# Optimization experiments

Measured on AMD Instinct MI355X. Metric: run time of the kernel, lower is better.

## Reference

```python
import jax, jax.numpy as jnp
import numpy as np

IN_FEATURES = 4096
OUT_FEATURES = 4096
N_GROUPS = 32
GROUP_SIZE = IN_FEATURES // N_GROUPS  # 128


def setup_inputs() -> dict:
    key = jax.random.key(0)
    k_x, k_qw, k_s, k_zp, k_b = jax.random.split(key, 5)
    x = jax.random.normal(k_x, (2, 2048, IN_FEATURES), dtype=jnp.float32)
    # 4-bit GPTQ quantized weight values in [0, 16)
    qweight_int = jax.random.randint(k_qw, (IN_FEATURES, OUT_FEATURES), 0, 16, dtype=jnp.int32)
    scales = jax.random.uniform(k_s, (N_GROUPS, OUT_FEATURES), dtype=jnp.float32, minval=0.001, maxval=0.02)
    zero_points = jax.random.randint(k_zp, (N_GROUPS, OUT_FEATURES), 0, 16, dtype=jnp.int32)
    # standard (non-permuted) g_idx: group index per input channel
    g_idx = (jnp.arange(IN_FEATURES, dtype=jnp.int32) // GROUP_SIZE).astype(jnp.int32)
    bias = jax.random.normal(k_b, (OUT_FEATURES,), dtype=jnp.float32)
    return {"x": x, "qweight_int": qweight_int, "scales": scales,
            "zero_points": zero_points, "g_idx": g_idx, "bias": bias}


def reference(x, qweight_int, scales, zero_points, g_idx, bias):
    dtype = x.dtype
    gi = g_idx.astype(jnp.int32)
    # dequantize: W[i, o] = scales[g_idx[i], o] * (q[i, o] - zp[g_idx[i], o])
    qw = qweight_int.astype(dtype)                       # [in, out]
    zp = zero_points.astype(dtype)[gi]                   # [in, out] via gather
    sc = scales.astype(dtype)[gi]                        # [in, out] via gather
    weight = sc * (qw - zp)                              # [in, out]
    out_shape = x.shape[:-1] + (qweight_int.shape[1],)
    x2d = x.reshape(-1, x.shape[-1])                     # [tokens, in]
    out = (x2d @ weight).reshape(out_shape)              # [b, s, out]
    out = out + bias.astype(dtype)
    return out
```

## Files before the change

### kernel.cpp

```cpp
#include <hip/hip_runtime.h>
#include <hip/hip_bf16.h>

typedef int  int4v  __attribute__((ext_vector_type(4)));
typedef int  int16v __attribute__((ext_vector_type(16)));

#define M_DIM 4096
#define N_DIM 4096
#define K_DIM 4096
#define NG 32
#define GS 128

__global__ void prep_kernel(const float* __restrict__ x,
                            signed char* __restrict__ xq,
                            float* __restrict__ sx,
                            const int* __restrict__ qw,
                            const int* __restrict__ zps,
                            signed char* __restrict__ wq) {
    __shared__ float red[4];
    __shared__ float inv_s;
    const int tid = threadIdx.x;
    if (blockIdx.x < 4096) {
        const int m = blockIdx.x;
        const float4* xr = reinterpret_cast<const float4*>(x + (long)m * K_DIM);
        float4 v[4];
        float amax = 0.f;
#pragma unroll
        for (int j = 0; j < 4; ++j) {
            v[j] = xr[tid * 4 + j];
            amax = fmaxf(amax, fmaxf(fmaxf(fabsf(v[j].x), fabsf(v[j].y)),
                                     fmaxf(fabsf(v[j].z), fabsf(v[j].w))));
        }
#pragma unroll
        for (int off = 32; off >= 1; off >>= 1)
            amax = fmaxf(amax, __shfl_xor(amax, off));
        if ((tid & 63) == 0) red[tid >> 6] = amax;
        __syncthreads();
        if (tid == 0) {
            float a = fmaxf(fmaxf(red[0], red[1]), fmaxf(red[2], red[3]));
            sx[m] = a * (1.f / 127.f);
            inv_s = (a > 0.f) ? 127.f / a : 0.f;
        }
        __syncthreads();
        const float inv = inv_s;
        unsigned p[4];
#pragma unroll
        for (int j = 0; j < 4; ++j) {
            int a0 = __float2int_rn(v[j].x * inv);
            int a1 = __float2int_rn(v[j].y * inv);
            int a2 = __float2int_rn(v[j].z * inv);
            int a3 = __float2int_rn(v[j].w * inv);
            p[j] = (a0 & 255) | ((a1 & 255) << 8) | ((a2 & 255) << 16) | ((a3 & 255) << 24);
        }
        *reinterpret_cast<uint4*>(xq + (long)m * K_DIM + tid * 16) =
            make_uint4(p[0], p[1], p[2], p[3]);
        return;
    }
    const int bx = blockIdx.x - 4096;
    const int n0 = (bx & 63) * 64;
    const int k0 = (bx >> 6) * 64;
    const int g  = k0 >> 7;
    const int n  = tid & 63;
    const int w  = tid >> 6;
    const int zp = zps[g * N_DIM + n0 + n];
    const int kk = k0 + w * 16;
    unsigned p[4];
#pragma unroll
    for (int c = 0; c < 4; ++c) {
        unsigned acc = 0;
#pragma unroll
        for (int j = 0; j < 4; ++j) {
            int q = qw[(long)(kk + c * 4 + j) * N_DIM + n0 + n];
            acc |= (unsigned)((q - zp) & 255) << (8 * j);
        }
        p[c] = acc;
    }
    *reinterpret_cast<uint4*>(wq + (long)(n0 + n) * K_DIM + kk) =
        make_uint4(p[0], p[1], p[2], p[3]);
}

#define BM 256
#define BN 128
#define BK 128

__device__ __forceinline__ void async_ld16(const signed char* g, const signed char* l) {
    __builtin_amdgcn_global_load_lds(
        (const __attribute__((address_space(1))) void*)g,
        (__attribute__((address_space(3))) void*)l, 16, 0, 0);
}

__global__ __launch_bounds__(256, 2) void gemm_kernel(
    const signed char* __restrict__ A,
    const signed char* __restrict__ Bq,
    const float* __restrict__ scales,
    const float* __restrict__ sx,
    const float* __restrict__ bias,
    float* __restrict__ C) {
    __shared__ signed char As[BM * BK];
    __shared__ signed char Bs[BN * BK];
    __shared__ float sS[NG * BN];
    __shared__ float sxs[BM];
    const int tid  = threadIdx.x;
    const int wave = tid >> 6;
    const int lane = tid & 63;
    const int half = lane >> 5;
    const int l32  = lane & 31;
    const int wm = (wave >> 1) * 128;
    const int wn = (wave & 1) * 64;
    const int m0 = blockIdx.y * BM;
    const int n0 = blockIdx.x * BN;

#pragma unroll
    for (int j = 0; j < 16; j += 4) {
        int i = tid * 16 + j;
        *reinterpret_cast<float4*>(&sS[i]) =
            *reinterpret_cast<const float4*>(&scales[(i >> 7) * N_DIM + n0 + (i & 127)]);
    }
    sxs[tid] = sx[m0 + tid];

    const int srow  = tid >> 3;
    const int sunit = (tid & 7) ^ (srow & 7);
    const signed char* agp = A  + (long)(m0 + srow) * K_DIM + sunit * 16;
    const signed char* bgp = Bq + (long)(n0 + srow) * K_DIM + sunit * 16;

    float facc[4][2][16];
#pragma unroll
    for (int mt = 0; mt < 4; ++mt)
#pragma unroll
        for (int nt = 0; nt < 2; ++nt)
#pragma unroll
            for (int r = 0; r < 16; ++r) facc[mt][nt][r] = 0.f;
    int16v zero16;
#pragma unroll
    for (int r = 0; r < 16; ++r) zero16[r] = 0;

    for (int kk = 0; kk < K_DIM; kk += BK) {
#pragma unroll
        for (int p = 0; p < 8; ++p)
            async_ld16(agp + (long)p * 32 * K_DIM + kk, As + p * 4096 + wave * 1024);
#pragma unroll
        for (int p = 0; p < 4; ++p)
            async_ld16(bgp + (long)p * 32 * K_DIM + kk, Bs + p * 4096 + wave * 1024);
        __syncthreads();
        const int g = kk >> 7;
        const float s0 = sS[g * BN + wn + l32];
        const float s1 = sS[g * BN + wn + 32 + l32];
        int4v bf[2][4];
#pragma unroll
        for (int nt = 0; nt < 2; ++nt) {
            int n = wn + nt * 32 + l32;
#pragma unroll
            for (int ks = 0; ks < 4; ++ks) {
                int slot = (2 * ks + half) ^ (n & 7);
                bf[nt][ks] = *reinterpret_cast<const int4v*>(&Bs[n * BK + slot * 16]);
            }
        }
#pragma unroll
        for (int mt = 0; mt < 4; ++mt) {
            int m = wm + mt * 32 + l32;
            int4v af[4];
#pragma unroll
            for (int ks = 0; ks < 4; ++ks) {
                int slot = (2 * ks + half) ^ (m & 7);
                af[ks] = *reinterpret_cast<const int4v*>(&As[m * BK + slot * 16]);
            }
            int16v c0 = __builtin_amdgcn_mfma_i32_32x32x32_i8(af[0], bf[0][0], zero16, 0, 0, 0);
            int16v c1 = __builtin_amdgcn_mfma_i32_32x32x32_i8(af[0], bf[1][0], zero16, 0, 0, 0);
#pragma unroll
            for (int ks = 1; ks < 4; ++ks) {
                c0 = __builtin_amdgcn_mfma_i32_32x32x32_i8(af[ks], bf[0][ks], c0, 0, 0, 0);
                c1 = __builtin_amdgcn_mfma_i32_32x32x32_i8(af[ks], bf[1][ks], c1, 0, 0, 0);
            }
#pragma unroll
            for (int r = 0; r < 16; ++r) {
                facc[mt][0][r] += s0 * (float)c0[r];
                facc[mt][1][r] += s1 * (float)c1[r];
            }
        }
        __syncthreads();
    }

    float bv[2];
    bv[0] = bias[n0 + wn + l32];
    bv[1] = bias[n0 + wn + 32 + l32];
    const int rowh = half * 4;
#pragma unroll
    for (int mt = 0; mt < 4; ++mt) {
#pragma unroll
        for (int r = 0; r < 16; ++r) {
            int row = (r & 3) + 8 * (r >> 2) + rowh;
            int gm  = m0 + wm + mt * 32 + row;
            float sxm = sxs[wm + mt * 32 + row];
            float* crow = C + (long)gm * N_DIM + n0 + wn;
            crow[l32]      = facc[mt][0][r] * sxm + bv[0];
            crow[32 + l32] = facc[mt][1][r] * sxm + bv[1];
        }
    }
}

extern "C" void kernel_launch(void* const* d_in, const int* in_sizes, int n_in,
                              void* d_out, int out_size, void* d_ws, size_t ws_size,
                              hipStream_t stream) {
    const float* x      = (const float*)d_in[0];
    const int*   qw     = (const int*)d_in[1];
    const float* scales = (const float*)d_in[2];
    const int*   zps    = (const int*)d_in[3];
    const float* bias   = (const float*)d_in[5];
    float* out = (float*)d_out;

    signed char* xq = (signed char*)d_ws;
    signed char* wq = (signed char*)d_ws + (size_t)M_DIM * K_DIM;
    float*       sx = (float*)((signed char*)d_ws + 2 * (size_t)M_DIM * K_DIM);

    prep_kernel<<<8192, 256, 0, stream>>>(x, xq, sx, qw, zps, wq);
    gemm_kernel<<<dim3(N_DIM / BN, M_DIM / BM), 256, 0, stream>>>(
        xq, wq, scales, sx, bias, out);
}
```

Baseline: 266.1 us.

## Double-buffer LDS tiles in 256x256 int8 GEMM with 512 threads and block swizzle

The int8 GEMM tile grows from 256x128 to 256x256 with 8 waves per block, and the A/B tiles are double-buffered in LDS so the async global-to-LDS loads for the next K step overlap the MFMA work on the current one. Per-group scales and the per-row activation scales are now read straight from global memory (scales prefetched one iteration ahead) instead of being staged in shared memory. Block indices are swizzled for L2 locality. LDS use rises to 128KB and occupancy drops to one block per CU, which trades latency hiding through concurrent blocks for deeper in-block pipelining. The prep kernel is unchanged and still accounts for part of the total time.

New measurement: 266.2 us. About the same (+0.0%).

```diff
diff --git a/kernel.cpp b/kernel.cpp
--- a/kernel.cpp
+++ b/kernel.cpp
@@ -79,8 +79,9 @@
 }
 
 #define BM 256
-#define BN 128
+#define BN 256
 #define BK 128
+#define NT (K_DIM / BK)
 
 __device__ __forceinline__ void async_ld16(const signed char* g, const signed char* l) {
     __builtin_amdgcn_global_load_lds(
@@ -88,39 +89,44 @@
         (__attribute__((address_space(3))) void*)l, 16, 0, 0);
 }
 
-__global__ __launch_bounds__(256, 2) void gemm_kernel(
+__device__ __forceinline__ void stage_tiles(const signed char* agp, const signed char* bgp,
+                                            signed char* asb, signed char* bsb,
+                                            int wave, int kk) {
+#pragma unroll
+    for (int p = 0; p < 4; ++p)
+        async_ld16(agp + (long)(p * 64) * K_DIM + kk, asb + p * 8192 + wave * 1024);
+#pragma unroll
+    for (int p = 0; p < 4; ++p)
+        async_ld16(bgp + (long)(p * 64) * K_DIM + kk, bsb + p * 8192 + wave * 1024);
+}
+
+__global__ __launch_bounds__(512, 1) void gemm_kernel(
     const signed char* __restrict__ A,
     const signed char* __restrict__ Bq,
     const float* __restrict__ scales,
     const float* __restrict__ sx,
     const float* __restrict__ bias,
     float* __restrict__ C) {
-    __shared__ signed char As[BM * BK];
-    __shared__ signed char Bs[BN * BK];
-    __shared__ float sS[NG * BN];
-    __shared__ float sxs[BM];
+    __shared__ signed char As[2][BM * BK];
+    __shared__ signed char Bs[2][BN * BK];
     const int tid  = threadIdx.x;
     const int wave = tid >> 6;
     const int lane = tid & 63;
     const int half = lane >> 5;
     const int l32  = lane & 31;
-    const int wm = (wave >> 1) * 128;
-    const int wn = (wave & 1) * 64;
-    const int m0 = blockIdx.y * BM;
-    const int n0 = blockIdx.x * BN;
-
-#pragma unroll
-    for (int j = 0; j < 16; j += 4) {
-        int i = tid * 16 + j;
-        *reinterpret_cast<float4*>(&sS[i]) =
-            *reinterpret_cast<const float4*>(&scales[(i >> 7) * N_DIM + n0 + (i & 127)]);
-    }
-    sxs[tid] = sx[m0 + tid];
+    const int wm = (wave >> 2) * 128;
+    const int wn = (wave & 3) * 64;
+
+    const int bid = (int)blockIdx.x;
+    const int swz = (bid & 7) * 32 + (bid >> 3);
+    const int m0 = (swz >> 4) * BM;
+    const int n0 = (swz & 15) * BN;
 
     const int srow  = tid >> 3;
     const int sunit = (tid & 7) ^ (srow & 7);
     const signed char* agp = A  + (long)(m0 + srow) * K_DIM + sunit * 16;
     const signed char* bgp = Bq + (long)(n0 + srow) * K_DIM + sunit * 16;
+    const float* sp = scales + n0 + wn + l32;
 
     float facc[4][2][16];
 #pragma unroll
@@ -133,17 +139,22 @@
 #pragma unroll
     for (int r = 0; r < 16; ++r) zero16[r] = 0;
 
-    for (int kk = 0; kk < K_DIM; kk += BK) {
-#pragma unroll
-        for (int p = 0; p < 8; ++p)
-            async_ld16(agp + (long)p * 32 * K_DIM + kk, As + p * 4096 + wave * 1024);
-#pragma unroll
-        for (int p = 0; p < 4; ++p)
-            async_ld16(bgp + (long)p * 32 * K_DIM + kk, Bs + p * 4096 + wave * 1024);
-        __syncthreads();
-        const int g = kk >> 7;
-        const float s0 = sS[g * BN + wn + l32];
-        const float s1 = sS[g * BN + wn + 32 + l32];
+    stage_tiles(agp, bgp, As[0], Bs[0], wave, 0);
+    float s0 = sp[0];
+    float s1 = sp[32];
+    __syncthreads();
+
+    for (int t = 0; t < NT; ++t) {
+        if (t + 1 < NT)
+            stage_tiles(agp, bgp, As[(t + 1) & 1], Bs[(t + 1) & 1], wave, (t + 1) * BK);
+        float ns0 = 0.f, ns1 = 0.f;
+        if (t + 1 < NT) {
+            ns0 = sp[(long)(t + 1) * N_DIM];
+            ns1 = sp[(long)(t + 1) * N_DIM + 32];
+        }
+
+        const signed char* Ab = As[t & 1];
+        const signed char* Bb = Bs[t & 1];
         int4v bf[2][4];
 #pragma unroll
         for (int nt = 0; nt < 2; ++nt) {
@@ -151,7 +162,7 @@
 #pragma unroll
             for (int ks = 0; ks < 4; ++ks) {
                 int slot = (2 * ks + half) ^ (n & 7);
-                bf[nt][ks] = *reinterpret_cast<const int4v*>(&Bs[n * BK + slot * 16]);
+                bf[nt][ks] = *reinterpret_cast<const int4v*>(&Bb[n * BK + slot * 16]);
             }
         }
 #pragma unroll
@@ -161,7 +172,7 @@
 #pragma unroll
             for (int ks = 0; ks < 4; ++ks) {
                 int slot = (2 * ks + half) ^ (m & 7);
-                af[ks] = *reinterpret_cast<const int4v*>(&As[m * BK + slot * 16]);
+                af[ks] = *reinterpret_cast<const int4v*>(&Ab[m * BK + slot * 16]);
             }
             int16v c0 = __builtin_amdgcn_mfma_i32_32x32x32_i8(af[0], bf[0][0], zero16, 0, 0, 0);
             int16v c1 = __builtin_amdgcn_mfma_i32_32x32x32_i8(af[0], bf[1][0], zero16, 0, 0, 0);
@@ -177,6 +188,8 @@
             }
         }
         __syncthreads();
+        s0 = ns0;
+        s1 = ns1;
     }
 
     float bv[2];
@@ -189,7 +202,7 @@
         for (int r = 0; r < 16; ++r) {
             int row = (r & 3) + 8 * (r >> 2) + rowh;
             int gm  = m0 + wm + mt * 32 + row;
-            float sxm = sxs[wm + mt * 32 + row];
+            float sxm = sx[gm];
             float* crow = C + (long)gm * N_DIM + n0 + wn;
             crow[l32]      = facc[mt][0][r] * sxm + bv[0];
             crow[32 + l32] = facc[mt][1][r] * sxm + bv[1];
@@ -212,6 +225,6 @@
     float*       sx = (float*)((signed char*)d_ws + 2 * (size_t)M_DIM * K_DIM);
 
     prep_kernel<<<8192, 256, 0, stream>>>(x, xq, sx, qw, zps, wq);
-    gemm_kernel<<<dim3(N_DIM / BN, M_DIM / BM), 256, 0, stream>>>(
+    gemm_kernel<<<N_DIM / BN * (M_DIM / BM), 512, 0, stream>>>(
         xq, wq, scales, sx, bias, out);
 }
```
